# Performance work log

Measured on AMD Instinct MI355X. Metric: run time of the kernel, lower is better.

## Reference

```python
import jax, jax.numpy as jnp
import numpy as np

N_NODES = 10000
N_EDGES = 640000
D = 128
BN_EPS = 1e-5


def setup_inputs() -> dict:
    key = jax.random.key(0)
    k1, k2, k3 = jax.random.split(key, 3)
    x = jax.random.normal(k1, (N_NODES, D), dtype=jnp.float32)
    edge_index = jax.random.randint(k2, (2, N_EDGES), 0, N_NODES, dtype=jnp.int64)
    W = jax.random.normal(k3, (D, D), dtype=jnp.float32) * (1.0 / np.sqrt(D))
    b = jnp.zeros((D,), dtype=jnp.float32)
    gamma = jnp.ones((D,), dtype=jnp.float32)
    beta = jnp.zeros((D,), dtype=jnp.float32)
    return {"x": x, "edge_index": edge_index, "W": W, "b": b, "gamma": gamma, "beta": beta}


def reference(x, edge_index, W, b, gamma, beta):
    # GINConv: out_i = MLP((1+eps)*x_i + sum_{j->i} x_j), eps=0
    src = edge_index[0]
    dst = edge_index[1]
    agg = jax.ops.segment_sum(x[src], dst, num_segments=N_NODES)  # [N, D]
    h = agg + x  # (1 + eps) * x with eps = 0
    # MLP inside GINConv: Linear + ReLU
    h = jnp.maximum(h @ W + b, 0.0)
    # outer F.relu (idempotent after inner ReLU, kept for faithfulness)
    h = jnp.maximum(h, 0.0)
    # BatchNorm1d, training-mode batch statistics (biased variance)
    mean = jnp.mean(h, axis=0)
    var = jnp.var(h, axis=0)
    h = (h - mean) * jax.lax.rsqrt(var + BN_EPS) * gamma + beta
    # Dropout in eval mode -> identity. his_x = [h]; return the main output.
    return h
```

## Files before the change

kernel.cpp:

```cpp
#include <hip/hip_runtime.h>

#define N_NODES 10000
#define N_EDGES 640000
#define D 128
#define BN_EPS 1e-5f
#define CAP 128
#define NSTRIPE 16
#define RPB 8
#define NB 313
#define BCAP 2400
#define ABLK 128
#define ASLICE 5000
#define CSENT 319

typedef _Float16 half4_t __attribute__((ext_vector_type(4)));
typedef unsigned short u16;

__global__ __launch_bounds__(256) void k_bin(
    const int* __restrict__ ei,
    const float4* __restrict__ x4,
    int* cur,
    int* __restrict__ recs,
    half4_t* __restrict__ xh)
{
    __shared__ int cnt[NB];
    __shared__ int base[NB];
    const int b = blockIdx.x, t = threadIdx.x;

    {
        const int n4 = N_NODES * D / 4;
        for (int i = b * 256 + t; i < n4; i += ABLK * 256) {
            const float4 v = x4[i];
            half4_t h;
            h.x = (_Float16)v.x; h.y = (_Float16)v.y;
            h.z = (_Float16)v.z; h.w = (_Float16)v.w;
            xh[i] = h;
        }
    }

    for (int i = t; i < NB; i += 256) cnt[i] = 0;
    __syncthreads();

    const int e0 = b * ASLICE;
    for (int i = t; i < ASLICE; i += 256)
        atomicAdd(&cnt[ei[N_EDGES + e0 + i] >> 5], 1);
    __syncthreads();

    const unsigned cbase = (unsigned)cur[CSENT];
    for (int i = t; i < NB; i += 256) {
        const int c = cnt[i];
        base[i] = (int)((unsigned)atomicAdd(&cur[i], c) - cbase);
        cnt[i] = 0;
    }
    __syncthreads();

    for (int i = t; i < ASLICE; i += 256) {
        const int e = e0 + i;
        const int d = ei[N_EDGES + e];
        const int s = ei[e];
        const int bin = d >> 5;
        const int p = base[bin] + atomicAdd(&cnt[bin], 1);
        if (p < BCAP) recs[bin * BCAP + p] = (s << 5) | (d & 31);
    }
}

__global__ __launch_bounds__(256) void k_fill(
    const int* __restrict__ recs,
    const int* __restrict__ cur,
    int* __restrict__ deg,
    u16* __restrict__ ssrc)
{
    __shared__ u16 lst[32 * CAP];
    __shared__ int cnt[32];
    const int bin = blockIdx.x, t = threadIdx.x;
    if (t < 32) cnt[t] = 0;
    __syncthreads();

    const unsigned cbase = (unsigned)cur[CSENT];
    int nrec = (int)((unsigned)cur[bin] - cbase);
    if (nrec > BCAP) nrec = BCAP;

    for (int i = t; i < nrec; i += 256) {
        const int r = recs[bin * BCAP + i];
        const int dl = r & 31;
        const int p = atomicAdd(&cnt[dl], 1);
        if (p < CAP) lst[dl * CAP + p] = (u16)(r >> 5);
    }
    __syncthreads();

    const int maxn = N_NODES - bin * 32;
    if (t < 32 && t < maxn)
        deg[bin * 32 + t] = min(cnt[t], CAP);

    const int4* s4 = (const int4*)lst;
    int4* d4 = (int4*)(ssrc + (size_t)bin * 32 * CAP);
    const int nch = (maxn >= 32) ? 512 : (maxn * CAP) / 8;
    for (int i = t; i < nch; i += 256) d4[i] = s4[i];
}

__global__ __launch_bounds__(256) void k_gmlp(
    const float* __restrict__ x,
    const half4_t* __restrict__ xh4,
    const int* __restrict__ deg,
    const u16* __restrict__ ssrc,
    const float* __restrict__ W,
    const float* __restrict__ bias,
    float* __restrict__ out,
    float* __restrict__ stats)
{
    __shared__ float hs[RPB][D];
    const int tid  = threadIdx.x;
    const int wv   = tid >> 6;
    const int lane = tid & 63;
    const int h    = lane >> 5;
    const int l    = lane & 31;
    const float4* __restrict__ x4 = (const float4*)x;

    #pragma unroll
    for (int j = 0; j < 2; j++) {
        const int lrow = wv * 2 + j;
        const int node = blockIdx.x * RPB + lrow;
        const int n = deg[node];
        const int off = node << 7;
        float4 acc = make_float4(0.f, 0.f, 0.f, 0.f);
        int i = 0;
        for (; i + 64 <= n; i += 64) {
            const int sj = (int)ssrc[off + i + lane];
            #pragma unroll
            for (int b = 0; b < 2; b++) {
                half4_t v[16];
                #pragma unroll
                for (int u = 0; u < 16; u++) {
                    const int p = b * 16 + u;
                    const int s = __shfl(sj, 2 * p + h, 64);
                    v[u] = xh4[(size_t)s * 32 + l];
                }
                #pragma unroll
                for (int u = 0; u < 16; u++) {
                    acc.x += (float)v[u].x; acc.y += (float)v[u].y;
                    acc.z += (float)v[u].z; acc.w += (float)v[u].w;
                }
            }
        }
        const int c = n - i;
        if (c > 0) {
            const int sj = (lane < c) ? (int)ssrc[off + i + lane] : 0;
            const int pairs = c >> 1;
            for (int t2 = 0; t2 < pairs; t2 += 16) {
                half4_t v[16];
                #pragma unroll
                for (int u = 0; u < 16; u++) {
                    const int s = __shfl(sj, (2 * (t2 + u) + h) & 63, 64);
                    v[u] = xh4[(size_t)s * 32 + l];
                }
                #pragma unroll
                for (int u = 0; u < 16; u++) {
                    if (t2 + u < pairs) {
                        acc.x += (float)v[u].x; acc.y += (float)v[u].y;
                        acc.z += (float)v[u].z; acc.w += (float)v[u].w;
                    }
                }
            }
            if (c & 1) {
                const int s = __shfl(sj, c - 1, 64);
                const half4_t vv = xh4[(size_t)s * 32 + l];
                if (h == 0) {
                    acc.x += (float)vv.x; acc.y += (float)vv.y;
                    acc.z += (float)vv.z; acc.w += (float)vv.w;
                }
            }
        }
        acc.x += __shfl_xor(acc.x, 32, 64);
        acc.y += __shfl_xor(acc.y, 32, 64);
        acc.z += __shfl_xor(acc.z, 32, 64);
        acc.w += __shfl_xor(acc.w, 32, 64);
        if (h == 0) {
            const float4 xv = x4[(size_t)node * 32 + l];
            float4 o;
            o.x = acc.x + xv.x; o.y = acc.y + xv.y;
            o.z = acc.z + xv.z; o.w = acc.w + xv.w;
            *(float4*)&hs[lrow][4 * l] = o;
        }
    }
    __syncthreads();

    const int col = tid & 127;
    const int rg  = tid >> 7;
    float a[4] = {0.f, 0.f, 0.f, 0.f};
    #pragma unroll 8
    for (int k = 0; k < D; k++) {
        const float w = W[k * D + col];
        #pragma unroll
        for (int r = 0; r < 4; r++)
            a[r] = fmaf(hs[rg * 4 + r][k], w, a[r]);
    }

    const float bcol = bias[col];
    float s1 = 0.f, s2 = 0.f;
    #pragma unroll
    for (int r = 0; r < 4; r++) {
        const float v = fmaxf(a[r] + bcol, 0.f);
        out[(size_t)(blockIdx.x * RPB + rg * 4 + r) * D + col] = v;
        s1 += v;
        s2 += v * v;
    }

    __syncthreads();
    float* red = &hs[0][0];
    red[tid]       = s1;
    red[256 + tid] = s2;
    __syncthreads();
    if (tid < D) {
        float* sp = &stats[(size_t)(blockIdx.x & (NSTRIPE - 1)) * 256];
        atomicAdd(&sp[tid],     red[tid]       + red[tid + 128]);
        atomicAdd(&sp[D + tid], red[256 + tid] + red[256 + tid + 128]);
    }
}

__global__ __launch_bounds__(256) void k_bn(
    float* out,
    const float* __restrict__ stats,
    const float* __restrict__ gamma,
    const float* __restrict__ beta)
{
    __shared__ float sc[D], sh[D];
    const int tid = threadIdx.x;
    if (tid < D) {
        const float fbase = stats[NSTRIPE * 256];
        float s = 0.f, q = 0.f;
        #pragma unroll
        for (int cp = 0; cp < NSTRIPE; cp++) {
            s += stats[cp * 256 + tid]     - fbase;
            q += stats[cp * 256 + D + tid] - fbase;
        }
        const float mean = s * (1.0f / N_NODES);
        const float var  = q * (1.0f / N_NODES) - mean * mean;
        const float scale = gamma[tid] * rsqrtf(var + BN_EPS);
        sc[tid] = scale;
        sh[tid] = beta[tid] - mean * scale;
    }
    __syncthreads();

    float4* o4 = (float4*)out;
    #pragma unroll
    for (int j = 0; j < 2; j++) {
        const int f = blockIdx.x * 512 + j * 256 + tid;
        const int c = (f & 31) << 2;
        float4 v = o4[f];
        v.x = v.x * sc[c]     + sh[c];
        v.y = v.y * sc[c + 1] + sh[c + 1];
        v.z = v.z * sc[c + 2] + sh[c + 2];
        v.w = v.w * sc[c + 3] + sh[c + 3];
        o4[f] = v;
    }
}

extern "C" void kernel_launch(void* const* d_in, const int* in_sizes, int n_in,
                              void* d_out, int out_size, void* d_ws, size_t ws_size,
                              hipStream_t stream)
{
    const float* x     = (const float*)d_in[0];
    const int*   ei    = (const int*)d_in[1];
    const float* W     = (const float*)d_in[2];
    const float* bias  = (const float*)d_in[3];
    const float* gamma = (const float*)d_in[4];
    const float* beta  = (const float*)d_in[5];
    float* out = (float*)d_out;

    int*     deg   = (int*)d_ws;
    float*   stats = (float*)(deg + 10240);
    int*     cur   = (int*)(stats + NSTRIPE * 256 + 8);
    int*     recs  = cur + 320;
    u16*     ssrc  = (u16*)(recs + NB * BCAP);
    half4_t* xh    = (half4_t*)(ssrc + (size_t)N_NODES * CAP);

    k_bin<<<ABLK, 256, 0, stream>>>(ei, (const float4*)x, cur, recs, xh);
    k_fill<<<NB, 256, 0, stream>>>(recs, cur, deg, ssrc);
    k_gmlp<<<N_NODES / RPB, 256, 0, stream>>>(x, xh, deg, ssrc, W, bias, out, stats);
    k_bn<<<N_NODES * D / 2048, 256, 0, stream>>>(out, stats, gamma, beta);
}
```

Measured before the change: 125.5 us.

## Fuse per-node adjacency fill into the gather-MLP kernel via shared-memory lists

Removes the separate k_fill kernel and its global ssrc/deg arrays. Each gather-MLP block now scans its 32-node bin's records directly and builds per-node source lists for its 8 nodes in shared memory. This cuts one launch and a global write plus reread of the adjacency lists. In exchange, each bin's records are read four times, once by each of the four blocks sharing that bin, and there is an extra sync before the gather.

```diff
diff --git a/kernel.cpp b/kernel.cpp
--- a/kernel.cpp
+++ b/kernel.cpp
@@ -64,68 +64,56 @@
     }
 }
 
-__global__ __launch_bounds__(256) void k_fill(
-    const int* __restrict__ recs,
-    const int* __restrict__ cur,
-    int* __restrict__ deg,
-    u16* __restrict__ ssrc)
-{
-    __shared__ u16 lst[32 * CAP];
-    __shared__ int cnt[32];
-    const int bin = blockIdx.x, t = threadIdx.x;
-    if (t < 32) cnt[t] = 0;
-    __syncthreads();
-
-    const unsigned cbase = (unsigned)cur[CSENT];
-    int nrec = (int)((unsigned)cur[bin] - cbase);
-    if (nrec > BCAP) nrec = BCAP;
-
-    for (int i = t; i < nrec; i += 256) {
-        const int r = recs[bin * BCAP + i];
-        const int dl = r & 31;
-        const int p = atomicAdd(&cnt[dl], 1);
-        if (p < CAP) lst[dl * CAP + p] = (u16)(r >> 5);
-    }
-    __syncthreads();
-
-    const int maxn = N_NODES - bin * 32;
-    if (t < 32 && t < maxn)
-        deg[bin * 32 + t] = min(cnt[t], CAP);
-
-    const int4* s4 = (const int4*)lst;
-    int4* d4 = (int4*)(ssrc + (size_t)bin * 32 * CAP);
-    const int nch = (maxn >= 32) ? 512 : (maxn * CAP) / 8;
-    for (int i = t; i < nch; i += 256) d4[i] = s4[i];
-}
-
-__global__ __launch_bounds__(256) void k_gmlp(
+__global__ __launch_bounds__(256) void k_gfill(
     const float* __restrict__ x,
     const half4_t* __restrict__ xh4,
-    const int* __restrict__ deg,
-    const u16* __restrict__ ssrc,
+    const int* __restrict__ cur,
+    const int* __restrict__ recs,
     const float* __restrict__ W,
     const float* __restrict__ bias,
     float* __restrict__ out,
     float* __restrict__ stats)
 {
+    __shared__ u16 lst[RPB * CAP];
+    __shared__ int cnt[RPB];
     __shared__ float hs[RPB][D];
     const int tid  = threadIdx.x;
+    const int bin  = blockIdx.x >> 2;
+    const int q    = blockIdx.x & 3;
     const int wv   = tid >> 6;
     const int lane = tid & 63;
     const int h    = lane >> 5;
     const int l    = lane & 31;
     const float4* __restrict__ x4 = (const float4*)x;
 
+    if (tid < RPB) cnt[tid] = 0;
+    __syncthreads();
+
+    const unsigned cbase = (unsigned)cur[CSENT];
+    int nrec = (int)((unsigned)cur[bin] - cbase);
+    if (nrec > BCAP) nrec = BCAP;
+    const int* __restrict__ br = recs + bin * BCAP;
+    for (int i = tid; i < nrec; i += 256) {
+        const int r = br[i];
+        const int dl = r & 31;
+        if ((dl >> 3) == q) {
+            const int p = atomicAdd(&cnt[dl & 7], 1);
+            if (p < CAP) lst[(dl & 7) * CAP + p] = (u16)(r >> 5);
+        }
+    }
+    __syncthreads();
+
     #pragma unroll
     for (int j = 0; j < 2; j++) {
         const int lrow = wv * 2 + j;
         const int node = blockIdx.x * RPB + lrow;
-        const int n = deg[node];
-        const int off = node << 7;
+        int n = cnt[lrow];
+        if (n > CAP) n = CAP;
+        const u16* __restrict__ myl = &lst[lrow * CAP];
         float4 acc = make_float4(0.f, 0.f, 0.f, 0.f);
         int i = 0;
         for (; i + 64 <= n; i += 64) {
-            const int sj = (int)ssrc[off + i + lane];
+            const int sj = (int)myl[i + lane];
             #pragma unroll
             for (int b = 0; b < 2; b++) {
                 half4_t v[16];
@@ -144,7 +132,7 @@
         }
         const int c = n - i;
         if (c > 0) {
-            const int sj = (lane < c) ? (int)ssrc[off + i + lane] : 0;
+            const int sj = (lane < c) ? (int)myl[i + lane] : 0;
             const int pairs = c >> 1;
             for (int t2 = 0; t2 < pairs; t2 += 16) {
                 half4_t v[16];
@@ -267,15 +255,12 @@
     const float* beta  = (const float*)d_in[5];
     float* out = (float*)d_out;
 
-    int*     deg   = (int*)d_ws;
-    float*   stats = (float*)(deg + 10240);
+    float*   stats = (float*)d_ws;
     int*     cur   = (int*)(stats + NSTRIPE * 256 + 8);
     int*     recs  = cur + 320;
-    u16*     ssrc  = (u16*)(recs + NB * BCAP);
-    half4_t* xh    = (half4_t*)(ssrc + (size_t)N_NODES * CAP);
+    half4_t* xh    = (half4_t*)(recs + NB * BCAP);
 
     k_bin<<<ABLK, 256, 0, stream>>>(ei, (const float4*)x, cur, recs, xh);
-    k_fill<<<NB, 256, 0, stream>>>(recs, cur, deg, ssrc);
-    k_gmlp<<<N_NODES / RPB, 256, 0, stream>>>(x, xh, deg, ssrc, W, bias, out, stats);
+    k_gfill<<<N_NODES / RPB, 256, 0, stream>>>(x, xh, cur, recs, W, bias, out, stats);
     k_bn<<<N_NODES * D / 2048, 256, 0, stream>>>(out, stats, gamma, beta);
 }
```

Result: faster. 122.6 us (-2.3%).
